# Kernel optimization log

Measured on AMD Instinct MI355X. Metric: run time of the kernel, lower is better.

The kernel has to match this reference:

```python
import jax, jax.numpy as jnp
import numpy as np

D_MODEL = 1024
NUM_HEADS = 16
DEPTH = D_MODEL // NUM_HEADS
MAX_LEN = 5000


def _make_pe(d_model=D_MODEL, max_len=MAX_LEN):
    # Faithful to torch PositionalEncoding: pe shape [max_len, 1, d_model]
    position = np.arange(max_len, dtype=np.float32)[:, None]
    div_term = np.exp(np.arange(0, d_model, 2, dtype=np.float32) * (-np.log(10000.0) / d_model))
    pe = np.zeros((max_len, d_model), dtype=np.float32)
    pe[:, 0::2] = np.sin(position * div_term)
    pe[:, 1::2] = np.cos(position * div_term)
    return jnp.asarray(pe[:, None, :])  # [max_len, 1, d_model]


def setup_inputs() -> dict:
    key = jax.random.key(0)
    ks = jax.random.split(key, 11)
    B, S, D = 4, 2048, D_MODEL
    s = 1.0 / np.sqrt(D)
    inp = {
        "v": jax.random.normal(ks[0], (B, S, D), jnp.float32),
        "k": jax.random.normal(ks[1], (B, S, D), jnp.float32),
        "q": jax.random.normal(ks[2], (B, S, D), jnp.float32),
        "wq_w": jax.random.normal(ks[3], (D, D), jnp.float32) * s,
        "wq_b": jnp.zeros((D,), jnp.float32),
        "wk_w": jax.random.normal(ks[4], (D, D), jnp.float32) * s,
        "wk_b": jnp.zeros((D,), jnp.float32),
        "wv_w": jax.random.normal(ks[5], (D, D), jnp.float32) * s,
        "wv_b": jnp.zeros((D,), jnp.float32),
        "dense_w": jax.random.normal(ks[6], (D, D), jnp.float32) * s,
        "dense_b": jnp.zeros((D,), jnp.float32),
        "pe": _make_pe(),
    }
    return inp


def _split_heads(x, B):
    # [B, S, D] -> [B, H, S, depth]
    return x.reshape(B, -1, NUM_HEADS, DEPTH).transpose(0, 2, 1, 3)


def reference(v, k, q, wq_w, wq_b, wk_w, wk_b, wv_w, wv_b, dense_w, dense_b, pe):
    B = q.shape[0]
    # Faithful bug-reproduction: pe[:batch] has shape [B, 1, D], broadcast over seq.
    pe_b = pe[:B]  # [B, 1, D]
    q = q + pe_b
    k = k + pe_b
    v = v + pe_b
    # Linear layers (torch: x @ W.T + b)
    qh = _split_heads(q @ wq_w.T + wq_b, B)  # [B,H,Sq,d]
    kh = _split_heads(k @ wk_w.T + wk_b, B)  # [B,H,Sk,d]
    vh = _split_heads(v @ wv_w.T + wv_b, B)  # [B,H,Sk,d]
    scale = 1.0 / jnp.sqrt(jnp.float32(DEPTH))
    logits = jnp.einsum("bhqd,bhkd->bhqk", qh, kh) * scale
    attn = jax.nn.softmax(logits, axis=-1)
    out = jnp.einsum("bhqk,bhkd->bhqd", attn, vh)
    out = out.transpose(0, 2, 1, 3).reshape(B, -1, D_MODEL)
    return out @ dense_w.T + dense_b
```

## Files before the change

kernel.cpp:

```cpp
#include <hip/hip_runtime.h>
#include <hip/hip_bf16.h>

typedef short short8 __attribute__((ext_vector_type(8)));
typedef float f32x4 __attribute__((ext_vector_type(4)));
typedef float f32x16 __attribute__((ext_vector_type(16)));
typedef unsigned int uint4v __attribute__((ext_vector_type(4)));

#define MFMA16(a, b, c) __builtin_amdgcn_mfma_f32_16x16x32_bf16(a, b, c, 0, 0, 0)
#define MFMA32(a, b, c) __builtin_amdgcn_mfma_f32_32x32x16_bf16(a, b, c, 0, 0, 0)

typedef __attribute__((address_space(1))) const unsigned int gas_u32;
typedef __attribute__((address_space(3))) unsigned int las_u32;

__device__ inline void gll16(const void* g, void* l) {
    __builtin_amdgcn_global_load_lds((gas_u32*)g, (las_u32*)l, 16, 0, 0);
}

__device__ inline unsigned short f2bf(float f) {
    unsigned u = __builtin_bit_cast(unsigned, f);
    u += 0x7fff + ((u >> 16) & 1);
    return (unsigned short)(u >> 16);
}

__device__ inline unsigned pk_perm(float a, float b, unsigned sel) {
    unsigned r;
    asm("v_perm_b32 %0, %1, %2, %3"
        : "=v"(r)
        : "v"(__builtin_bit_cast(unsigned, b)), "v"(__builtin_bit_cast(unsigned, a)), "s"(sel));
    return r;
}

__device__ inline float exp2_fast(float x) {
#if __has_builtin(__builtin_amdgcn_exp2f)
    return __builtin_amdgcn_exp2f(x);
#else
    float r; asm("v_exp_f32 %0, %1" : "=v"(r) : "v"(x)); return r;
#endif
}

__device__ inline void pl32_swap(unsigned &a, unsigned &b) {
    asm volatile("v_permlane32_swap_b32 %0, %1" : "+v"(a), "+v"(b));
}

__global__ void pe_cast3(const float* __restrict__ q, const float* __restrict__ k,
                         const float* __restrict__ v, const float* __restrict__ pe,
                         unsigned short* __restrict__ oq, unsigned short* __restrict__ ok,
                         unsigned short* __restrict__ ov) {
    const float* x = (blockIdx.y == 0) ? q : (blockIdx.y == 1) ? k : v;
    unsigned short* o = (blockIdx.y == 0) ? oq : (blockIdx.y == 1) ? ok : ov;
    int i = blockIdx.x * 256 + threadIdx.x;
    long e = (long)i * 4;
    int b = (int)(e >> 21);
    int d = (int)(e & 1023);
    float4 xv = reinterpret_cast<const float4*>(x)[i];
    float4 pv = *reinterpret_cast<const float4*>(pe + b * 1024 + d);
    ushort4 r;
    r.x = f2bf(xv.x + pv.x); r.y = f2bf(xv.y + pv.y);
    r.z = f2bf(xv.z + pv.z); r.w = f2bf(xv.w + pv.w);
    reinterpret_cast<ushort4*>(o)[i] = r;
}

__global__ void wcast4(const float* __restrict__ w0, const float* __restrict__ w1,
                       const float* __restrict__ w2, const float* __restrict__ w3,
                       unsigned short* __restrict__ o0) {
    const float* w = (blockIdx.y == 0) ? w0 : (blockIdx.y == 1) ? w1
                   : (blockIdx.y == 2) ? w2 : w3;
    unsigned short* o = o0 + (size_t)blockIdx.y * 1024 * 1024;
    int i = blockIdx.x * 256 + threadIdx.x;
    float4 xv = reinterpret_cast<const float4*>(w)[i];
    ushort4 r;
    r.x = f2bf(xv.x); r.y = f2bf(xv.y); r.z = f2bf(xv.z); r.w = f2bf(xv.w);
    reinterpret_cast<ushort4*>(o)[i] = r;
}

template <int MF, int MODE>
__global__ __launch_bounds__(512, 2) void gemm4(const unsigned short* __restrict__ A0,
                                                const unsigned short* __restrict__ W0,
                                                const float* __restrict__ bq,
                                                const float* __restrict__ bk,
                                                const float* __restrict__ bv,
                                                void* __restrict__ oq,
                                                void* __restrict__ ok,
                                                void* __restrict__ ov,
                                                float qscale) {
    const int NT = 16;
    const int BM = MF * 32;
    constexpr int AR = BM / 64;
    __shared__ __align__(16) unsigned short lsA[2][BM * 64];
    __shared__ __align__(16) unsigned short lsB[2][256 * 64];

    int z = (MODE == 3) ? blockIdx.z : 0;
    const unsigned short* A = A0 + (size_t)z * 8192 * 1024;
    const unsigned short* W = W0 + (size_t)z * 1024 * 1024;
    const float* bias = (MODE == 3) ? ((z == 0) ? bq : (z == 1) ? bk : bv) : bq;
    float scale = (MODE == 3 && z == 0) ? qscale : 1.0f;

    int tid = threadIdx.x, wave = tid >> 6, lane = tid & 63;
    int lg = lane >> 4, l15 = lane & 15;
    int wr = wave >> 2, wc = wave & 3;
    int brow = blockIdx.x * BM;
    int bcol = blockIdx.y * 256;

    int srow = tid >> 3;
    int scol = ((tid ^ srow) & 7) * 8;
    const unsigned short* pA = A + (long)(brow + srow) * 1024 + scol;
    const unsigned short* pB = W + (long)(bcol + srow) * 1024 + scol;

    f32x4 acc[MF][4];
#pragma unroll
    for (int m = 0; m < MF; ++m)
#pragma unroll
        for (int n = 0; n < 4; ++n) acc[m][n] = f32x4{0.f, 0.f, 0.f, 0.f};

#define STG_A(t, bi) do {                                                   \
        _Pragma("unroll")                                                   \
        for (int j = 0; j < AR; ++j)                                        \
            gll16(pA + (t) * 64 + j * 65536,                                \
                  (char*)lsA[bi] + (j * 512 + wave * 64) * 16);             \
    } while (0)
#define STG_B(t, bi) do {                                                   \
        _Pragma("unroll")                                                   \
        for (int j = 0; j < 4; ++j)                                         \
            gll16(pB + (t) * 64 + j * 65536,                                \
                  (char*)lsB[bi] + (j * 512 + wave * 64) * 16);             \
    } while (0)

    STG_A(0, 0);
    STG_B(0, 0);
    asm volatile("s_waitcnt vmcnt(0)" ::: "memory");
    __syncthreads();

    int swz = (l15 & 7) << 4;
    for (int t = 0; t < NT; ++t) {
        int cb = t & 1;
        const char* KA = (const char*)lsA[cb];
        const char* KB = (const char*)lsB[cb];

        if (t < NT - 1) STG_A(t + 1, cb ^ 1);

        short8 af0[4][2], bf0[2][2];
#pragma unroll
        for (int m = 0; m < 4; ++m)
#pragma unroll
            for (int kk = 0; kk < 2; ++kk) {
                int row = wr * (MF * 16) + m * 16 + l15;
                af0[m][kk] = *(const short8*)(KA + row * 128 + (((kk * 4 + lg) << 4) ^ swz));
            }
#pragma unroll
        for (int n = 0; n < 2; ++n)
#pragma unroll
            for (int kk = 0; kk < 2; ++kk) {
                int row = wc * 64 + n * 16 + l15;
                bf0[n][kk] = *(const short8*)(KB + row * 128 + (((kk * 4 + lg) << 4) ^ swz));
            }
        __builtin_amdgcn_s_setprio(1);
#pragma unroll
        for (int m = 0; m < 4; ++m)
#pragma unroll
            for (int n = 0; n < 2; ++n)
#pragma unroll
                for (int kk = 0; kk < 2; ++kk)
                    acc[m][n] = MFMA16(af0[m][kk], bf0[n][kk], acc[m][n]);
        __builtin_amdgcn_s_setprio(0);

        if (t < NT - 1) STG_B(t + 1, cb ^ 1);

        short8 bf1[2][2];
#pragma unroll
        for (int n = 0; n < 2; ++n)
#pragma unroll
            for (int kk = 0; kk < 2; ++kk) {
                int row = wc * 64 + (n + 2) * 16 + l15;
                bf1[n][kk] = *(const short8*)(KB + row * 128 + (((kk * 4 + lg) << 4) ^ swz));
            }
        __builtin_amdgcn_s_setprio(1);
#pragma unroll
        for (int m = 0; m < 4; ++m)
#pragma unroll
            for (int n = 0; n < 2; ++n)
#pragma unroll
                for (int kk = 0; kk < 2; ++kk)
                    acc[m][n + 2] = MFMA16(af0[m][kk], bf1[n][kk], acc[m][n + 2]);
        __builtin_amdgcn_s_setprio(0);

        if (MF == 8) {
            short8 af1[4][2];
#pragma unroll
            for (int m = 0; m < 4; ++m)
#pragma unroll
                for (int kk = 0; kk < 2; ++kk) {
                    int row = wr * (MF * 16) + (m + 4) * 16 + l15;
                    af1[m][kk] = *(const short8*)(KA + row * 128 + (((kk * 4 + lg) << 4) ^ swz));
                }
            __builtin_amdgcn_s_setprio(1);
#pragma unroll
            for (int m = 0; m < 4; ++m)
#pragma unroll
                for (int n = 0; n < 2; ++n)
#pragma unroll
                    for (int kk = 0; kk < 2; ++kk)
                        acc[m + 4][n] = MFMA16(af1[m][kk], bf0[n][kk], acc[m + 4][n]);
#pragma unroll
            for (int m = 0; m < 4; ++m)
#pragma unroll
                for (int n = 0; n < 2; ++n)
#pragma unroll
                    for (int kk = 0; kk < 2; ++kk)
                        acc[m + 4][n + 2] = MFMA16(af1[m][kk], bf1[n][kk], acc[m + 4][n + 2]);
            __builtin_amdgcn_s_setprio(0);
        }

        asm volatile("s_waitcnt vmcnt(0)" ::: "memory");
        __syncthreads();
    }
#undef STG_A
#undef STG_B

    void* out = (MODE == 3) ? ((z == 0) ? oq : (z == 1) ? ok : ov) : oq;
#pragma unroll
    for (int m = 0; m < MF; ++m)
#pragma unroll
        for (int n = 0; n < 4; ++n) {
            int col = bcol + wc * 64 + n * 16 + l15;
            float bv_ = bias[col];
            int row0 = brow + wr * (MF * 16) + m * 16 + lg * 4;
            if (MODE == 3 && z == 2) {
                int b = row0 >> 11, s0 = row0 & 2047;
                ushort4 pk;
                pk.x = f2bf(acc[m][n][0] + bv_);
                pk.y = f2bf(acc[m][n][1] + bv_);
                pk.z = f2bf(acc[m][n][2] + bv_);
                pk.w = f2bf(acc[m][n][3] + bv_);
                *(ushort4*)((unsigned short*)out + ((long)(b * 1024 + col)) * 2048 + s0) = pk;
            } else {
#pragma unroll
                for (int r = 0; r < 4; ++r) {
                    int row = row0 + r;
                    float v = (acc[m][n][r] + bv_) * scale;
                    if (MODE == 1) {
                        ((float*)out)[(long)row * 1024 + col] = v;
                    } else {
                        int b = row >> 11, s = row & 2047, h = col >> 6, d = col & 63;
                        ((unsigned short*)out)[(((long)(b * 16 + h) * 2048 + s) * 64 + d)] = f2bf(v);
                    }
                }
            }
        }
}

__global__ __launch_bounds__(256, 2) void attn_kernel(const unsigned short* __restrict__ Qh,
                                                      const unsigned short* __restrict__ Kh,
                                                      const unsigned short* __restrict__ Vt,
                                                      unsigned short* __restrict__ Om) {
    const int S = 2048;
    const int NT = S / 64;
    int flat = blockIdx.x;
    int nf_ = (flat & 7) * 64 + (flat >> 3);
    int qt = nf_ & 7;
    int bh = nf_ >> 3;
    int b = bh >> 4, h = bh & 15;

    int tid = threadIdx.x, wave = tid >> 6, lane = tid & 63;
    int l31 = lane & 31, hi = lane >> 5;

    __shared__ __align__(16) unsigned short Kl[3][4096];
    __shared__ __align__(16) unsigned short Vtl[3][4096];

    const unsigned short* Qb = Qh + (long)bh * S * 64;
    const unsigned short* Kb = Kh + (long)bh * S * 64;
    const unsigned short* Vb = Vt + (long)bh * 64 * S;

    int colS = ((((tid & 7) * 16) ^ (((tid >> 3) & 7) << 4)) >> 1);
    const unsigned short* srcK = Kb + (tid >> 3) * 64 + colS;
    const unsigned short* srcV = Vb + (tid >> 3) * 2048 + colS;

    short8 aq[2][4];
    {
        const unsigned short* qrow = Qb + (long)(qt * 256 + wave * 64 + l31) * 64 + hi * 8;
#pragma unroll
        for (int qf = 0; qf < 2; ++qf)
#pragma unroll
            for (int s = 0; s < 4; ++s)
                aq[qf][s] = *(const short8*)(qrow + qf * 32 * 64 + s * 16);
    }

    f32x16 oacc[2][2], lacc[2], z16;
#pragma unroll
    for (int r = 0; r < 16; ++r) {
        oacc[0][0][r] = 0.f; oacc[0][1][r] = 0.f;
        oacc[1][0][r] = 0.f; oacc[1][1][r] = 0.f;
        lacc[0][r] = 0.f; lacc[1][r] = 0.f;
        z16[r] = 0.f;
    }

    const short8 ones8 = {0x3F80, 0x3F80, 0x3F80, 0x3F80, 0x3F80, 0x3F80, 0x3F80, 0x3F80};
    const unsigned SEL = 0x07060302u;

    int rb0 = l31 * 128;
    int swz = (l31 & 7) << 4;

#define STAGE(kt, bi) do {                                              \
        const unsigned short* sk = srcK + (kt) * 4096;                  \
        gll16(sk,         (char*)Kl[bi] + wave * 1024);                 \
        gll16(sk + 2048,  (char*)Kl[bi] + 4096 + wave * 1024);          \
        const unsigned short* sv = srcV + (kt) * 64;                    \
        gll16(sv,         (char*)Vtl[bi] + wave * 1024);                \
        gll16(sv + 65536, (char*)Vtl[bi] + 4096 + wave * 1024);         \
    } while (0)

    STAGE(0, 0);
    STAGE(1, 1);

    int bi = 0, sb = 2;
    for (int kt = 0; kt < NT; ++kt) {
        if (kt == NT - 1) { asm volatile("s_waitcnt vmcnt(0)" ::: "memory"); }
        else              { asm volatile("s_waitcnt vmcnt(4)" ::: "memory"); }
        __builtin_amdgcn_s_barrier();
        if (kt < NT - 2) STAGE(kt + 2, sb);

        const char* KlC = (const char*)Kl[bi];
        const char* VlC = (const char*)Vtl[bi];

        f32x16 sacc[2][2];
        __builtin_amdgcn_s_setprio(1);
#pragma unroll
        for (int blk = 0; blk < 2; ++blk) {
            short8 kf0 = *(const short8*)(KlC + blk * 4096 + rb0 + ((16 * hi) ^ swz));
            sacc[0][blk] = MFMA32(kf0, aq[0][0], z16);
            sacc[1][blk] = MFMA32(kf0, aq[1][0], z16);
#pragma unroll
            for (int s = 1; s < 4; ++s) {
                short8 kf = *(const short8*)(KlC + blk * 4096 + rb0 + ((32 * s + 16 * hi) ^ swz));
                sacc[0][blk] = MFMA32(kf, aq[0][s], sacc[0][blk]);
                sacc[1][blk] = MFMA32(kf, aq[1][s], sacc[1][blk]);
            }
        }
        __builtin_amdgcn_s_setprio(0);

#pragma unroll
        for (int qf = 0; qf < 2; ++qf)
#pragma unroll
            for (int blk = 0; blk < 2; ++blk)
#pragma unroll
                for (int r = 0; r < 16; ++r) sacc[qf][blk][r] = exp2_fast(sacc[qf][blk][r]);

#pragma unroll
        for (int s = 0; s < 4; ++s) {
            const int blk = s >> 1, base = (s & 1) * 8;
            short8 pa[2];
#pragma unroll
            for (int qf = 0; qf < 2; ++qf) {
                unsigned q0 = pk_perm(sacc[qf][blk][base + 0], sacc[qf][blk][base + 1], SEL);
                unsigned q1 = pk_perm(sacc[qf][blk][base + 2], sacc[qf][blk][base + 3], SEL);
                unsigned q2 = pk_perm(sacc[qf][blk][base + 4], sacc[qf][blk][base + 5], SEL);
                unsigned q3 = pk_perm(sacc[qf][blk][base + 6], sacc[qf][blk][base + 7], SEL);
                pl32_swap(q0, q2);
                pl32_swap(q1, q3);
                uint4v pw; pw[0] = q0; pw[1] = q1; pw[2] = q2; pw[3] = q3;
                pa[qf] = __builtin_bit_cast(short8, pw);
            }
            __builtin_amdgcn_s_setprio(1);
#pragma unroll
            for (int dblk = 0; dblk < 2; ++dblk) {
                short8 vf = *(const short8*)(VlC + dblk * 4096 + rb0 + ((32 * s + 16 * hi) ^ swz));
                oacc[0][dblk] = MFMA32(pa[0], vf, oacc[0][dblk]);
                oacc[1][dblk] = MFMA32(pa[1], vf, oacc[1][dblk]);
            }
            lacc[0] = MFMA32(pa[0], ones8, lacc[0]);
            lacc[1] = MFMA32(pa[1], ones8, lacc[1]);
            __builtin_amdgcn_s_setprio(0);
        }
        bi = (bi == 2) ? 0 : bi + 1;
        sb = (sb == 2) ? 0 : sb + 1;
    }
#undef STAGE

#pragma unroll
    for (int qf = 0; qf < 2; ++qf) {
        float inv[16];
#pragma unroll
        for (int r = 0; r < 16; ++r) inv[r] = 1.0f / lacc[qf][r];
        int qrow0 = qt * 256 + wave * 64 + qf * 32 + 4 * hi;
#pragma unroll
        for (int dblk = 0; dblk < 2; ++dblk)
#pragma unroll
            for (int r = 0; r < 16; ++r) {
                int qrow = qrow0 + (r & 3) + 8 * (r >> 2);
                int d = h * 64 + dblk * 32 + l31;
                float v = oacc[qf][dblk][r] * inv[r];
                Om[((long)b * 2048 + qrow) * 1024 + d] = f2bf(v);
            }
    }
}

extern "C" void kernel_launch(void* const* d_in, const int* in_sizes, int n_in,
                              void* d_out, int out_size, void* d_ws, size_t ws_size,
                              hipStream_t stream) {
    const float* v_in = (const float*)d_in[0];
    const float* k_in = (const float*)d_in[1];
    const float* q_in = (const float*)d_in[2];
    const float* wq_w = (const float*)d_in[3];
    const float* wq_b = (const float*)d_in[4];
    const float* wk_w = (const float*)d_in[5];
    const float* wk_b = (const float*)d_in[6];
    const float* wv_w = (const float*)d_in[7];
    const float* wv_b = (const float*)d_in[8];
    const float* wd_w = (const float*)d_in[9];
    const float* wd_b = (const float*)d_in[10];
    const float* pe   = (const float*)d_in[11];

    const long SZ = 8192L * 1024 * 2;
    char* ws = (char*)d_ws;
    unsigned short* xq = (unsigned short*)(ws + 0);
    unsigned short* xk = (unsigned short*)(ws + SZ);
    unsigned short* xv = (unsigned short*)(ws + 2 * SZ);
    unsigned short* qh = (unsigned short*)(ws + 3 * SZ);
    unsigned short* kh = (unsigned short*)(ws + 4 * SZ);
    unsigned short* vt = (unsigned short*)(ws + 5 * SZ);
    unsigned short* wqb16 = (unsigned short*)(ws + 6 * SZ);

    pe_cast3<<<dim3(8192, 3), 256, 0, stream>>>(q_in, k_in, v_in, pe, xq, xk, xv);
    wcast4<<<dim3(1024, 4), 256, 0, stream>>>(wq_w, wk_w, wv_w, wd_w, wqb16);

    const float QSCALE = 0.125f * 1.44269504088896f;
    gemm4<8, 3><<<dim3(32, 4, 3), 512, 0, stream>>>(
        xq, wqb16, wq_b, wk_b, wv_b, qh, kh, vt, QSCALE);

    unsigned short* om = xq;
    attn_kernel<<<512, 256, 0, stream>>>(qh, kh, vt, om);

    gemm4<4, 1><<<dim3(64, 4, 1), 512, 0, stream>>>(
        om, wqb16 + 3L * 1024 * 1024, wd_b, nullptr, nullptr, d_out, nullptr, nullptr, 1.0f);
}
```

Baseline: 217.0 us.

## Split QKV GEMM staging into quarter-tile loads with finer-grained waitcnt barriers

The fused QKV projection GEMM is specialized and its prefetch of the next K-tile is split into four pairs of global-to-LDS loads. Each pair is issued after a separate barrier inside the MFMA phases, and partial vmcnt waits replace the full drain plus __syncthreads at the end of each iteration. The goal is to overlap global loads with compute more evenly and avoid the full pipeline stall per K-step. The dense output GEMM keeps the old schedule as a separate non-templated kernel. The per-quarter barriers and the vmcnt counts must exactly match the order in which the loads land, or stale LDS data could be read.

```diff
diff --git a/kernel.cpp b/kernel.cpp
--- a/kernel.cpp
+++ b/kernel.cpp
@@ -73,8 +73,7 @@
     reinterpret_cast<ushort4*>(o)[i] = r;
 }
 
-template <int MF, int MODE>
-__global__ __launch_bounds__(512, 2) void gemm4(const unsigned short* __restrict__ A0,
+__global__ __launch_bounds__(512, 2) void gemm5(const unsigned short* __restrict__ A0,
                                                 const unsigned short* __restrict__ W0,
                                                 const float* __restrict__ bq,
                                                 const float* __restrict__ bk,
@@ -84,21 +83,19 @@
                                                 void* __restrict__ ov,
                                                 float qscale) {
     const int NT = 16;
-    const int BM = MF * 32;
-    constexpr int AR = BM / 64;
-    __shared__ __align__(16) unsigned short lsA[2][BM * 64];
+    __shared__ __align__(16) unsigned short lsA[2][256 * 64];
     __shared__ __align__(16) unsigned short lsB[2][256 * 64];
 
-    int z = (MODE == 3) ? blockIdx.z : 0;
+    int z = blockIdx.z;
     const unsigned short* A = A0 + (size_t)z * 8192 * 1024;
     const unsigned short* W = W0 + (size_t)z * 1024 * 1024;
-    const float* bias = (MODE == 3) ? ((z == 0) ? bq : (z == 1) ? bk : bv) : bq;
-    float scale = (MODE == 3 && z == 0) ? qscale : 1.0f;
+    const float* bias = (z == 0) ? bq : (z == 1) ? bk : bv;
+    float scale = (z == 0) ? qscale : 1.0f;
 
     int tid = threadIdx.x, wave = tid >> 6, lane = tid & 63;
     int lg = lane >> 4, l15 = lane & 15;
     int wr = wave >> 2, wc = wave & 3;
-    int brow = blockIdx.x * BM;
+    int brow = blockIdx.x * 256;
     int bcol = blockIdx.y * 256;
 
     int srow = tid >> 3;
@@ -106,53 +103,42 @@
     const unsigned short* pA = A + (long)(brow + srow) * 1024 + scol;
     const unsigned short* pB = W + (long)(bcol + srow) * 1024 + scol;
 
-    f32x4 acc[MF][4];
-#pragma unroll
-    for (int m = 0; m < MF; ++m)
+    f32x4 acc[8][4];
+#pragma unroll
+    for (int m = 0; m < 8; ++m)
 #pragma unroll
         for (int n = 0; n < 4; ++n) acc[m][n] = f32x4{0.f, 0.f, 0.f, 0.f};
 
-#define STG_A(t, bi) do {                                                   \
-        _Pragma("unroll")                                                   \
-        for (int j = 0; j < AR; ++j)                                        \
-            gll16(pA + (t) * 64 + j * 65536,                                \
-                  (char*)lsA[bi] + (j * 512 + wave * 64) * 16);             \
-    } while (0)
-#define STG_B(t, bi) do {                                                   \
-        _Pragma("unroll")                                                   \
-        for (int j = 0; j < 4; ++j)                                         \
-            gll16(pB + (t) * 64 + j * 65536,                                \
-                  (char*)lsB[bi] + (j * 512 + wave * 64) * 16);             \
-    } while (0)
-
-    STG_A(0, 0);
-    STG_B(0, 0);
-    asm volatile("s_waitcnt vmcnt(0)" ::: "memory");
-    __syncthreads();
+#define STG_A(t, bi, q) gll16(pA + (t) * 64 + (q) * 65536,                    \
+                              (char*)lsA[bi] + ((q) * 512 + wave * 64) * 16)
+#define STG_B(t, bi, q) gll16(pB + (t) * 64 + (q) * 65536,                    \
+                              (char*)lsB[bi] + ((q) * 512 + wave * 64) * 16)
+
+    STG_B(0, 0, 0); STG_B(0, 0, 1); STG_B(0, 0, 2); STG_B(0, 0, 3);
+    STG_A(0, 0, 0); STG_A(0, 0, 2); STG_A(0, 0, 1); STG_A(0, 0, 3);
 
     int swz = (l15 & 7) << 4;
     for (int t = 0; t < NT; ++t) {
-        int cb = t & 1;
+        int cb = t & 1, nb = cb ^ 1;
         const char* KA = (const char*)lsA[cb];
         const char* KB = (const char*)lsB[cb];
-
-        if (t < NT - 1) STG_A(t + 1, cb ^ 1);
-
-        short8 af0[4][2], bf0[2][2];
-#pragma unroll
-        for (int m = 0; m < 4; ++m)
-#pragma unroll
-            for (int kk = 0; kk < 2; ++kk) {
-                int row = wr * (MF * 16) + m * 16 + l15;
-                af0[m][kk] = *(const short8*)(KA + row * 128 + (((kk * 4 + lg) << 4) ^ swz));
-            }
+        short8 af0[4][2], af1[4][2], bf0[2][2], bf1[2][2];
+
+        asm volatile("s_waitcnt vmcnt(2)" ::: "memory");
+        __builtin_amdgcn_s_barrier();
+        if (t < NT - 1) { STG_B(t + 1, nb, 0); STG_B(t + 1, nb, 1); }
+#pragma unroll
+        for (int m = 0; m < 4; ++m)
+#pragma unroll
+            for (int kk = 0; kk < 2; ++kk)
+                af0[m][kk] = *(const short8*)(KA + (wr * 128 + m * 16 + l15) * 128 +
+                                              (((kk * 4 + lg) << 4) ^ swz));
 #pragma unroll
         for (int n = 0; n < 2; ++n)
 #pragma unroll
-            for (int kk = 0; kk < 2; ++kk) {
-                int row = wc * 64 + n * 16 + l15;
-                bf0[n][kk] = *(const short8*)(KB + row * 128 + (((kk * 4 + lg) << 4) ^ swz));
-            }
+            for (int kk = 0; kk < 2; ++kk)
+                bf0[n][kk] = *(const short8*)(KB + (wc * 64 + n * 16 + l15) * 128 +
+                                              (((kk * 4 + lg) << 4) ^ swz));
         __builtin_amdgcn_s_setprio(1);
 #pragma unroll
         for (int m = 0; m < 4; ++m)
@@ -163,16 +149,14 @@
                     acc[m][n] = MFMA16(af0[m][kk], bf0[n][kk], acc[m][n]);
         __builtin_amdgcn_s_setprio(0);
 
-        if (t < NT - 1) STG_B(t + 1, cb ^ 1);
-
-        short8 bf1[2][2];
+        __builtin_amdgcn_s_barrier();
+        if (t < NT - 1) { STG_B(t + 1, nb, 2); STG_B(t + 1, nb, 3); }
 #pragma unroll
         for (int n = 0; n < 2; ++n)
 #pragma unroll
-            for (int kk = 0; kk < 2; ++kk) {
-                int row = wc * 64 + (n + 2) * 16 + l15;
-                bf1[n][kk] = *(const short8*)(KB + row * 128 + (((kk * 4 + lg) << 4) ^ swz));
-            }
+            for (int kk = 0; kk < 2; ++kk)
+                bf1[n][kk] = *(const short8*)(KB + (wc * 64 + (n + 2) * 16 + l15) * 128 +
+                                              (((kk * 4 + lg) << 4) ^ swz));
         __builtin_amdgcn_s_setprio(1);
 #pragma unroll
         for (int m = 0; m < 4; ++m)
@@ -183,48 +167,50 @@
                     acc[m][n + 2] = MFMA16(af0[m][kk], bf1[n][kk], acc[m][n + 2]);
         __builtin_amdgcn_s_setprio(0);
 
-        if (MF == 8) {
-            short8 af1[4][2];
-#pragma unroll
-            for (int m = 0; m < 4; ++m)
-#pragma unroll
-                for (int kk = 0; kk < 2; ++kk) {
-                    int row = wr * (MF * 16) + (m + 4) * 16 + l15;
-                    af1[m][kk] = *(const short8*)(KA + row * 128 + (((kk * 4 + lg) << 4) ^ swz));
-                }
-            __builtin_amdgcn_s_setprio(1);
-#pragma unroll
-            for (int m = 0; m < 4; ++m)
-#pragma unroll
-                for (int n = 0; n < 2; ++n)
-#pragma unroll
-                    for (int kk = 0; kk < 2; ++kk)
-                        acc[m + 4][n] = MFMA16(af1[m][kk], bf0[n][kk], acc[m + 4][n]);
-#pragma unroll
-            for (int m = 0; m < 4; ++m)
-#pragma unroll
-                for (int n = 0; n < 2; ++n)
-#pragma unroll
-                    for (int kk = 0; kk < 2; ++kk)
-                        acc[m + 4][n + 2] = MFMA16(af1[m][kk], bf1[n][kk], acc[m + 4][n + 2]);
-            __builtin_amdgcn_s_setprio(0);
-        }
-
-        asm volatile("s_waitcnt vmcnt(0)" ::: "memory");
-        __syncthreads();
+        if (t == NT - 1) { asm volatile("s_waitcnt vmcnt(0)" ::: "memory"); }
+        else             { asm volatile("s_waitcnt vmcnt(4)" ::: "memory"); }
+        __builtin_amdgcn_s_barrier();
+        if (t < NT - 1) { STG_A(t + 1, nb, 0); STG_A(t + 1, nb, 2); }
+#pragma unroll
+        for (int m = 0; m < 4; ++m)
+#pragma unroll
+            for (int kk = 0; kk < 2; ++kk)
+                af1[m][kk] = *(const short8*)(KA + (wr * 128 + (m + 4) * 16 + l15) * 128 +
+                                              (((kk * 4 + lg) << 4) ^ swz));
+        __builtin_amdgcn_s_setprio(1);
+#pragma unroll
+        for (int m = 0; m < 4; ++m)
+#pragma unroll
+            for (int n = 0; n < 2; ++n)
+#pragma unroll
+                for (int kk = 0; kk < 2; ++kk)
+                    acc[m + 4][n] = MFMA16(af1[m][kk], bf0[n][kk], acc[m + 4][n]);
+        __builtin_amdgcn_s_setprio(0);
+
+        __builtin_amdgcn_s_barrier();
+        if (t < NT - 1) { STG_A(t + 1, nb, 1); STG_A(t + 1, nb, 3); }
+        __builtin_amdgcn_s_setprio(1);
+#pragma unroll
+        for (int m = 0; m < 4; ++m)
+#pragma unroll
+            for (int n = 0; n < 2; ++n)
+#pragma unroll
+                for (int kk = 0; kk < 2; ++kk)
+                    acc[m + 4][n + 2] = MFMA16(af1[m][kk], bf1[n][kk], acc[m + 4][n + 2]);
+        __builtin_amdgcn_s_setprio(0);
     }
 #undef STG_A
 #undef STG_B
 
-    void* out = (MODE == 3) ? ((z == 0) ? oq : (z == 1) ? ok : ov) : oq;
-#pragma unroll
-    for (int m = 0; m < MF; ++m)
+    void* out = (z == 0) ? oq : (z == 1) ? ok : ov;
+#pragma unroll
+    for (int m = 0; m < 8; ++m)
 #pragma unroll
         for (int n = 0; n < 4; ++n) {
             int col = bcol + wc * 64 + n * 16 + l15;
             float bv_ = bias[col];
-            int row0 = brow + wr * (MF * 16) + m * 16 + lg * 4;
-            if (MODE == 3 && z == 2) {
+            int row0 = brow + wr * 128 + m * 16 + lg * 4;
+            if (z == 2) {
                 int b = row0 >> 11, s0 = row0 & 2047;
                 ushort4 pk;
                 pk.x = f2bf(acc[m][n][0] + bv_);
@@ -237,13 +223,125 @@
                 for (int r = 0; r < 4; ++r) {
                     int row = row0 + r;
                     float v = (acc[m][n][r] + bv_) * scale;
-                    if (MODE == 1) {
-                        ((float*)out)[(long)row * 1024 + col] = v;
-                    } else {
-                        int b = row >> 11, s = row & 2047, h = col >> 6, d = col & 63;
-                        ((unsigned short*)out)[(((long)(b * 16 + h) * 2048 + s) * 64 + d)] = f2bf(v);
-                    }
+                    int b = row >> 11, s = row & 2047, h = col >> 6, d = col & 63;
+                    ((unsigned short*)out)[(((long)(b * 16 + h) * 2048 + s) * 64 + d)] = f2bf(v);
                 }
+            }
+        }
+}
+
+__global__ __launch_bounds__(512, 2) void gemm_dense(const unsigned short* __restrict__ A,
+                                                     const unsigned short* __restrict__ W,
+                                                     const float* __restrict__ bias,
+                                                     float* __restrict__ out) {
+    const int NT = 16;
+    __shared__ __align__(16) unsigned short lsA[2][128 * 64];
+    __shared__ __align__(16) unsigned short lsB[2][256 * 64];
+
+    int tid = threadIdx.x, wave = tid >> 6, lane = tid & 63;
+    int lg = lane >> 4, l15 = lane & 15;
+    int wr = wave >> 2, wc = wave & 3;
+    int brow = blockIdx.x * 128;
+    int bcol = blockIdx.y * 256;
+
+    int srow = tid >> 3;
+    int scol = ((tid ^ srow) & 7) * 8;
+    const unsigned short* pA = A + (long)(brow + srow) * 1024 + scol;
+    const unsigned short* pB = W + (long)(bcol + srow) * 1024 + scol;
+
+    f32x4 acc[4][4];
+#pragma unroll
+    for (int m = 0; m < 4; ++m)
+#pragma unroll
+        for (int n = 0; n < 4; ++n) acc[m][n] = f32x4{0.f, 0.f, 0.f, 0.f};
+
+#define STG_A(t, bi) do {                                                     \
+        _Pragma("unroll")                                                     \
+        for (int j = 0; j < 2; ++j)                                           \
+            gll16(pA + (t) * 64 + j * 65536,                                  \
+                  (char*)lsA[bi] + (j * 512 + wave * 64) * 16);               \
+    } while (0)
+#define STG_B(t, bi) do {                                                     \
+        _Pragma("unroll")                                                     \
+        for (int j = 0; j < 4; ++j)                                           \
+            gll16(pB + (t) * 64 + j * 65536,                                  \
+                  (char*)lsB[bi] + (j * 512 + wave * 64) * 16);               \
+    } while (0)
+
+    STG_A(0, 0);
+    STG_B(0, 0);
+    asm volatile("s_waitcnt vmcnt(0)" ::: "memory");
+    __syncthreads();
+
+    int swz = (l15 & 7) << 4;
+    for (int t = 0; t < NT; ++t) {
+        int cb = t & 1;
+        const char* KA = (const char*)lsA[cb];
+        const char* KB = (const char*)lsB[cb];
+
+        if (t < NT - 1) STG_A(t + 1, cb ^ 1);
+
+        short8 af0[4][2], bf0[2][2];
+#pragma unroll
+        for (int m = 0; m < 4; ++m)
+#pragma unroll
+            for (int kk = 0; kk < 2; ++kk) {
+                int row = wr * 64 + m * 16 + l15;
+                af0[m][kk] = *(const short8*)(KA + row * 128 + (((kk * 4 + lg) << 4) ^ swz));
+            }
+#pragma unroll
+        for (int n = 0; n < 2; ++n)
+#pragma unroll
+            for (int kk = 0; kk < 2; ++kk) {
+                int row = wc * 64 + n * 16 + l15;
+                bf0[n][kk] = *(const short8*)(KB + row * 128 + (((kk * 4 + lg) << 4) ^ swz));
+            }
+        __builtin_amdgcn_s_setprio(1);
+#pragma unroll
+        for (int m = 0; m < 4; ++m)
+#pragma unroll
+            for (int n = 0; n < 2; ++n)
+#pragma unroll
+                for (int kk = 0; kk < 2; ++kk)
+                    acc[m][n] = MFMA16(af0[m][kk], bf0[n][kk], acc[m][n]);
+        __builtin_amdgcn_s_setprio(0);
+
+        if (t < NT - 1) STG_B(t + 1, cb ^ 1);
+
+        short8 bf1[2][2];
+#pragma unroll
+        for (int n = 0; n < 2; ++n)
+#pragma unroll
+            for (int kk = 0; kk < 2; ++kk) {
+                int row = wc * 64 + (n + 2) * 16 + l15;
+                bf1[n][kk] = *(const short8*)(KB + row * 128 + (((kk * 4 + lg) << 4) ^ swz));
+            }
+        __builtin_amdgcn_s_setprio(1);
+#pragma unroll
+        for (int m = 0; m < 4; ++m)
+#pragma unroll
+            for (int n = 0; n < 2; ++n)
+#pragma unroll
+                for (int kk = 0; kk < 2; ++kk)
+                    acc[m][n + 2] = MFMA16(af0[m][kk], bf1[n][kk], acc[m][n + 2]);
+        __builtin_amdgcn_s_setprio(0);
+
+        asm volatile("s_waitcnt vmcnt(0)" ::: "memory");
+        __syncthreads();
+    }
+#undef STG_A
+#undef STG_B
+
+#pragma unroll
+    for (int m = 0; m < 4; ++m)
+#pragma unroll
+        for (int n = 0; n < 4; ++n) {
+            int col = bcol + wc * 64 + n * 16 + l15;
+            float bv_ = bias[col];
+#pragma unroll
+            for (int r = 0; r < 4; ++r) {
+                int row = brow + wr * 64 + m * 16 + lg * 4 + r;
+                out[(long)row * 1024 + col] = acc[m][n][r] + bv_;
             }
         }
 }
@@ -423,12 +521,12 @@
     wcast4<<<dim3(1024, 4), 256, 0, stream>>>(wq_w, wk_w, wv_w, wd_w, wqb16);
 
     const float QSCALE = 0.125f * 1.44269504088896f;
-    gemm4<8, 3><<<dim3(32, 4, 3), 512, 0, stream>>>(
+    gemm5<<<dim3(32, 4, 3), 512, 0, stream>>>(
         xq, wqb16, wq_b, wk_b, wv_b, qh, kh, vt, QSCALE);
 
     unsigned short* om = xq;
     attn_kernel<<<512, 256, 0, stream>>>(qh, kh, vt, om);
 
-    gemm4<4, 1><<<dim3(64, 4, 1), 512, 0, stream>>>(
-        om, wqb16 + 3L * 1024 * 1024, wd_b, nullptr, nullptr, d_out, nullptr, nullptr, 1.0f);
-}
+    gemm_dense<<<dim3(64, 4), 512, 0, stream>>>(
+        om, wqb16 + 3L * 1024 * 1024, wd_b, (float*)d_out);
+}
```

New measurement: 229.1 us. 1.06x slower.

## Interleave tile prefetch with MFMA phases using partial waitcnts in 256x256 GEMM

Applied to the files above, without the earlier changes.

The GEMM kernel is rewritten as a fixed 256x256-tile variant. Its global-to-LDS prefetch is split into quarter-tile chunks issued between four MFMA phases, with barriers and partial vmcnt waits replacing the single full wait and syncthreads at the end of each k-step. The output projection now also uses 256-row tiles, which halves its grid to 128 blocks. The aim is to hide load latency behind compute. The cost is more barriers per iteration and fewer blocks for the output GEMM on a large GPU.

```diff
diff --git a/kernel.cpp b/kernel.cpp
--- a/kernel.cpp
+++ b/kernel.cpp
@@ -73,8 +73,8 @@
     reinterpret_cast<ushort4*>(o)[i] = r;
 }
 
-template <int MF, int MODE>
-__global__ __launch_bounds__(512, 2) void gemm4(const unsigned short* __restrict__ A0,
+template <int MODE>
+__global__ __launch_bounds__(512, 2) void gemm8(const unsigned short* __restrict__ A0,
                                                 const unsigned short* __restrict__ W0,
                                                 const float* __restrict__ bq,
                                                 const float* __restrict__ bk,
@@ -84,9 +84,7 @@
                                                 void* __restrict__ ov,
                                                 float qscale) {
     const int NT = 16;
-    const int BM = MF * 32;
-    constexpr int AR = BM / 64;
-    __shared__ __align__(16) unsigned short lsA[2][BM * 64];
+    __shared__ __align__(16) unsigned short lsA[2][256 * 64];
     __shared__ __align__(16) unsigned short lsB[2][256 * 64];
 
     int z = (MODE == 3) ? blockIdx.z : 0;
@@ -98,7 +96,7 @@
     int tid = threadIdx.x, wave = tid >> 6, lane = tid & 63;
     int lg = lane >> 4, l15 = lane & 15;
     int wr = wave >> 2, wc = wave & 3;
-    int brow = blockIdx.x * BM;
+    int brow = blockIdx.x * 256;
     int bcol = blockIdx.y * 256;
 
     int srow = tid >> 3;
@@ -106,53 +104,45 @@
     const unsigned short* pA = A + (long)(brow + srow) * 1024 + scol;
     const unsigned short* pB = W + (long)(bcol + srow) * 1024 + scol;
 
-    f32x4 acc[MF][4];
-#pragma unroll
-    for (int m = 0; m < MF; ++m)
+    f32x4 acc[8][4];
+#pragma unroll
+    for (int m = 0; m < 8; ++m)
 #pragma unroll
         for (int n = 0; n < 4; ++n) acc[m][n] = f32x4{0.f, 0.f, 0.f, 0.f};
 
-#define STG_A(t, bi) do {                                                   \
-        _Pragma("unroll")                                                   \
-        for (int j = 0; j < AR; ++j)                                        \
-            gll16(pA + (t) * 64 + j * 65536,                                \
-                  (char*)lsA[bi] + (j * 512 + wave * 64) * 16);             \
-    } while (0)
-#define STG_B(t, bi) do {                                                   \
-        _Pragma("unroll")                                                   \
-        for (int j = 0; j < 4; ++j)                                         \
-            gll16(pB + (t) * 64 + j * 65536,                                \
-                  (char*)lsB[bi] + (j * 512 + wave * 64) * 16);             \
-    } while (0)
-
-    STG_A(0, 0);
-    STG_B(0, 0);
-    asm volatile("s_waitcnt vmcnt(0)" ::: "memory");
-    __syncthreads();
-
-    int swz = (l15 & 7) << 4;
+#define SA(t, bi, q) gll16(pA + (t) * 64 + (q) * 65536,                     \
+                           (char*)lsA[bi] + ((q) * 512 + wave * 64) * 16)
+#define SB(t, bi, q) gll16(pB + (t) * 64 + (q) * 65536,                     \
+                           (char*)lsB[bi] + ((q) * 512 + wave * 64) * 16)
+
+    SB(0, 0, 0); SB(0, 0, 1); SB(0, 0, 2); SB(0, 0, 3);
+    SA(0, 0, 0); SA(0, 0, 2); SA(0, 0, 1); SA(0, 0, 3);
+    asm volatile("s_waitcnt vmcnt(2)" ::: "memory");
+    __builtin_amdgcn_s_barrier();
+
+    int swz_ = (l15 & 7) << 4;
     for (int t = 0; t < NT; ++t) {
-        int cb = t & 1;
+        int cb = t & 1, nb = cb ^ 1;
         const char* KA = (const char*)lsA[cb];
         const char* KB = (const char*)lsB[cb];
-
-        if (t < NT - 1) STG_A(t + 1, cb ^ 1);
-
-        short8 af0[4][2], bf0[2][2];
-#pragma unroll
-        for (int m = 0; m < 4; ++m)
-#pragma unroll
-            for (int kk = 0; kk < 2; ++kk) {
-                int row = wr * (MF * 16) + m * 16 + l15;
-                af0[m][kk] = *(const short8*)(KA + row * 128 + (((kk * 4 + lg) << 4) ^ swz));
-            }
+        short8 af0[4][2], af1[4][2], bf0[2][2], bf1[2][2];
+        const bool st = (t < NT - 1);
+
+#pragma unroll
+        for (int m = 0; m < 4; ++m)
+#pragma unroll
+            for (int kk = 0; kk < 2; ++kk)
+                af0[m][kk] = *(const short8*)(KA + (wr * 128 + m * 16 + l15) * 128 +
+                                              (((kk * 4 + lg) << 4) ^ swz_));
 #pragma unroll
         for (int n = 0; n < 2; ++n)
 #pragma unroll
-            for (int kk = 0; kk < 2; ++kk) {
-                int row = wc * 64 + n * 16 + l15;
-                bf0[n][kk] = *(const short8*)(KB + row * 128 + (((kk * 4 + lg) << 4) ^ swz));
-            }
+            for (int kk = 0; kk < 2; ++kk)
+                bf0[n][kk] = *(const short8*)(KB + (wc * 64 + n * 16 + l15) * 128 +
+                                              (((kk * 4 + lg) << 4) ^ swz_));
+        if (st) { SB(t + 1, nb, 0); SB(t + 1, nb, 1); }
+        __builtin_amdgcn_s_barrier();
+        asm volatile("s_waitcnt lgkmcnt(0)" ::: "memory");
         __builtin_amdgcn_s_setprio(1);
 #pragma unroll
         for (int m = 0; m < 4; ++m)
@@ -162,17 +152,19 @@
                 for (int kk = 0; kk < 2; ++kk)
                     acc[m][n] = MFMA16(af0[m][kk], bf0[n][kk], acc[m][n]);
         __builtin_amdgcn_s_setprio(0);
-
-        if (t < NT - 1) STG_B(t + 1, cb ^ 1);
-
-        short8 bf1[2][2];
+        __builtin_amdgcn_s_barrier();
+
 #pragma unroll
         for (int n = 0; n < 2; ++n)
 #pragma unroll
-            for (int kk = 0; kk < 2; ++kk) {
-                int row = wc * 64 + (n + 2) * 16 + l15;
-                bf1[n][kk] = *(const short8*)(KB + row * 128 + (((kk * 4 + lg) << 4) ^ swz));
-            }
+            for (int kk = 0; kk < 2; ++kk)
+                bf1[n][kk] = *(const short8*)(KB + (wc * 64 + (n + 2) * 16 + l15) * 128 +
+                                              (((kk * 4 + lg) << 4) ^ swz_));
+        if (st) { SB(t + 1, nb, 2); SB(t + 1, nb, 3); }
+        if (st) { asm volatile("s_waitcnt vmcnt(4)" ::: "memory"); }
+        else    { asm volatile("s_waitcnt vmcnt(0)" ::: "memory"); }
+        __builtin_amdgcn_s_barrier();
+        asm volatile("s_waitcnt lgkmcnt(0)" ::: "memory");
         __builtin_amdgcn_s_setprio(1);
 #pragma unroll
         for (int m = 0; m < 4; ++m)
@@ -182,48 +174,55 @@
                 for (int kk = 0; kk < 2; ++kk)
                     acc[m][n + 2] = MFMA16(af0[m][kk], bf1[n][kk], acc[m][n + 2]);
         __builtin_amdgcn_s_setprio(0);
-
-        if (MF == 8) {
-            short8 af1[4][2];
-#pragma unroll
-            for (int m = 0; m < 4; ++m)
-#pragma unroll
-                for (int kk = 0; kk < 2; ++kk) {
-                    int row = wr * (MF * 16) + (m + 4) * 16 + l15;
-                    af1[m][kk] = *(const short8*)(KA + row * 128 + (((kk * 4 + lg) << 4) ^ swz));
-                }
-            __builtin_amdgcn_s_setprio(1);
-#pragma unroll
-            for (int m = 0; m < 4; ++m)
-#pragma unroll
-                for (int n = 0; n < 2; ++n)
-#pragma unroll
-                    for (int kk = 0; kk < 2; ++kk)
-                        acc[m + 4][n] = MFMA16(af1[m][kk], bf0[n][kk], acc[m + 4][n]);
-#pragma unroll
-            for (int m = 0; m < 4; ++m)
-#pragma unroll
-                for (int n = 0; n < 2; ++n)
-#pragma unroll
-                    for (int kk = 0; kk < 2; ++kk)
-                        acc[m + 4][n + 2] = MFMA16(af1[m][kk], bf1[n][kk], acc[m + 4][n + 2]);
-            __builtin_amdgcn_s_setprio(0);
+        __builtin_amdgcn_s_barrier();
+
+#pragma unroll
+        for (int m = 0; m < 4; ++m)
+#pragma unroll
+            for (int kk = 0; kk < 2; ++kk)
+                af1[m][kk] = *(const short8*)(KA + (wr * 128 + (m + 4) * 16 + l15) * 128 +
+                                              (((kk * 4 + lg) << 4) ^ swz_));
+        if (st) { SA(t + 1, nb, 0); SA(t + 1, nb, 2); }
+        __builtin_amdgcn_s_barrier();
+        asm volatile("s_waitcnt lgkmcnt(0)" ::: "memory");
+        __builtin_amdgcn_s_setprio(1);
+#pragma unroll
+        for (int m = 0; m < 4; ++m)
+#pragma unroll
+            for (int n = 0; n < 2; ++n)
+#pragma unroll
+                for (int kk = 0; kk < 2; ++kk)
+                    acc[m + 4][n] = MFMA16(af1[m][kk], bf0[n][kk], acc[m + 4][n]);
+        __builtin_amdgcn_s_setprio(0);
+        __builtin_amdgcn_s_barrier();
+
+        if (st) {
+            SA(t + 1, nb, 1); SA(t + 1, nb, 3);
+            asm volatile("s_waitcnt vmcnt(2)" ::: "memory");
         }
-
-        asm volatile("s_waitcnt vmcnt(0)" ::: "memory");
-        __syncthreads();
+        __builtin_amdgcn_s_barrier();
+        __builtin_amdgcn_s_setprio(1);
+#pragma unroll
+        for (int m = 0; m < 4; ++m)
+#pragma unroll
+            for (int n = 0; n < 2; ++n)
+#pragma unroll
+                for (int kk = 0; kk < 2; ++kk)
+                    acc[m + 4][n + 2] = MFMA16(af1[m][kk], bf1[n][kk], acc[m + 4][n + 2]);
+        __builtin_amdgcn_s_setprio(0);
+        __builtin_amdgcn_s_barrier();
     }
-#undef STG_A
-#undef STG_B
+#undef SA
+#undef SB
 
     void* out = (MODE == 3) ? ((z == 0) ? oq : (z == 1) ? ok : ov) : oq;
 #pragma unroll
-    for (int m = 0; m < MF; ++m)
+    for (int m = 0; m < 8; ++m)
 #pragma unroll
         for (int n = 0; n < 4; ++n) {
             int col = bcol + wc * 64 + n * 16 + l15;
             float bv_ = bias[col];
-            int row0 = brow + wr * (MF * 16) + m * 16 + lg * 4;
+            int row0 = brow + wr * 128 + m * 16 + lg * 4;
             if (MODE == 3 && z == 2) {
                 int b = row0 >> 11, s0 = row0 & 2047;
                 ushort4 pk;
@@ -423,12 +422,12 @@
     wcast4<<<dim3(1024, 4), 256, 0, stream>>>(wq_w, wk_w, wv_w, wd_w, wqb16);
 
     const float QSCALE = 0.125f * 1.44269504088896f;
-    gemm4<8, 3><<<dim3(32, 4, 3), 512, 0, stream>>>(
+    gemm8<3><<<dim3(32, 4, 3), 512, 0, stream>>>(
         xq, wqb16, wq_b, wk_b, wv_b, qh, kh, vt, QSCALE);
 
     unsigned short* om = xq;
     attn_kernel<<<512, 256, 0, stream>>>(qh, kh, vt, om);
 
-    gemm4<4, 1><<<dim3(64, 4, 1), 512, 0, stream>>>(
+    gemm8<1><<<dim3(32, 4, 1), 512, 0, stream>>>(
         om, wqb16 + 3L * 1024 * 1024, wd_b, nullptr, nullptr, d_out, nullptr, nullptr, 1.0f);
 }
```

Measured after the change: 216.1 us. Within noise of the previous version (-0.4%).
